# Performance work log

Hardware: AMD Instinct MI355X
Metric: run time of the kernel (lower is better)

The kernel has to match this reference:

```python
import jax, jax.numpy as jnp
import numpy as np

T, D, N, K, H = 2048, 4096, 32, 8, 128
ROPE_THETA = 500000.0


def setup_inputs() -> dict:
    key = jax.random.key(0)
    ks = jax.random.split(key, 5)
    s = 0.02
    return {
        "x": jax.random.normal(ks[0], (T, D), jnp.float32) * s,
        "positions": jnp.arange(T, dtype=jnp.int64 if jax.config.jax_enable_x64 else jnp.int32),
        "Wq": jax.random.normal(ks[1], (D, N, H), jnp.float32) * s,
        "Wk": jax.random.normal(ks[2], (D, K, H), jnp.float32) * s,
        "Wv": jax.random.normal(ks[3], (D, K, H), jnp.float32) * s,
        "Wo": jax.random.normal(ks[4], (N, H, D), jnp.float32) * s,
    }


def _rope(positions, q, k):
    # positions: [T]; q: [T,N,H]; k: [T,K,H]. Half-split rotation (Llama style).
    half = H // 2
    inv_freq = 1.0 / (ROPE_THETA ** (jnp.arange(0, half, dtype=jnp.float32) / half))
    ang = positions.astype(jnp.float32)[:, None] * inv_freq  # [T, H/2]
    cos = jnp.cos(ang)[:, None, :]  # [T,1,H/2]
    sin = jnp.sin(ang)[:, None, :]

    def rot(x):
        x1, x2 = x[..., :half], x[..., half:]
        return jnp.concatenate([x1 * cos - x2 * sin, x2 * cos + x1 * sin], axis=-1)

    return rot(q), rot(k)


def reference(x, positions, Wq, Wk, Wv, Wo):
    q = jnp.einsum('td,dnh->tnh', x, Wq)  # [T,N,H]
    k = jnp.einsum('td,dkh->tkh', x, Wk)  # [T,K,H]
    v = jnp.einsum('td,dkh->tkh', x, Wv)
    q, k = _rope(positions, q, k)

    rep = N // K  # GQA: expand kv heads to query heads
    kr = jnp.repeat(k, rep, axis=1)  # [T,N,H]
    vr = jnp.repeat(v, rep, axis=1)

    scale = 1.0 / jnp.sqrt(jnp.asarray(H, jnp.float32))
    scores = jnp.einsum('tnh,snh->nts', q, kr) * scale  # [N,T,T]
    causal = positions[:, None] >= positions[None, :]   # [T,T]
    scores = jnp.where(causal[None, :, :], scores, jnp.finfo(scores.dtype).min)
    probs = jax.nn.softmax(scores, axis=-1)
    ctx = jnp.einsum('nts,snh->tnh', probs, vr)  # [T,N,H]
    return jnp.einsum('tnh,nhd->td', ctx, Wo)
```

## Files before the change

### kernel.cpp

```cpp
#include <hip/hip_runtime.h>
#include <hip/hip_bf16.h>

#define T_SEQ 2048
#define D_MODEL 4096
#define N_HEADS 32
#define K_HEADS 8
#define HEAD_DIM 128

typedef unsigned short u16;
typedef short sfrag8 __attribute__((ext_vector_type(8)));
typedef float ffrag4 __attribute__((ext_vector_type(4)));

#if defined(__has_builtin)
#  if __has_builtin(__builtin_amdgcn_exp2f)
#    define EXP2F(x) __builtin_amdgcn_exp2f(x)
#  else
#    define EXP2F(x) exp2f(x)
#  endif
#else
#  define EXP2F(x) exp2f(x)
#endif

#define QSCALE_LOG2E 0.12751744900463627f

__device__ __forceinline__ float bf2f(u16 u) {
    return __uint_as_float(((unsigned int)u) << 16);
}
__device__ __forceinline__ u16 f2bf(float f) {
    unsigned int x = __float_as_uint(f);
    unsigned int r = (x + 0x7fffu + ((x >> 16) & 1u)) >> 16;
    return (u16)r;
}
__device__ __forceinline__ uint4 pack8(const float4 a, const float4 b) {
    uint4 r;
    r.x = (unsigned)f2bf(a.x) | ((unsigned)f2bf(a.y) << 16);
    r.y = (unsigned)f2bf(a.z) | ((unsigned)f2bf(a.w) << 16);
    r.z = (unsigned)f2bf(b.x) | ((unsigned)f2bf(b.y) << 16);
    r.w = (unsigned)f2bf(b.z) | ((unsigned)f2bf(b.w) << 16);
    return r;
}

__device__ __forceinline__ void gload_lds16(const u16* g, u16* l) {
    __builtin_amdgcn_global_load_lds(
        (const __attribute__((address_space(1))) void*)g,
        (__attribute__((address_space(3))) void*)l, 16, 0, 0);
}

__global__ __launch_bounds__(256) void convert_bf16(
    const float* __restrict__ X, u16* __restrict__ Y, int n8)
{
    const int i = blockIdx.x * 256 + threadIdx.x;
    if (i < n8) {
        float4 a = ((const float4*)X)[(size_t)i * 2];
        float4 b = ((const float4*)X)[(size_t)i * 2 + 1];
        ((uint4*)Y)[i] = pack8(a, b);
    }
}

__global__ __launch_bounds__(256) void transpose_f32_bf16(
    const float* __restrict__ W, u16* __restrict__ WT, int R, int C)
{
    __shared__ float Ts[64][65];
    const int t = threadIdx.x;
    const int c0 = blockIdx.x * 64, r0 = blockIdx.y * 64;
    const int rl = t >> 4, cl = (t & 15) * 4;
#pragma unroll
    for (int p = 0; p < 4; ++p) {
        const int r = p * 16 + rl;
        float4 v = *(const float4*)(W + (size_t)(r0 + r) * C + c0 + cl);
        Ts[r][cl] = v.x; Ts[r][cl + 1] = v.y; Ts[r][cl + 2] = v.z; Ts[r][cl + 3] = v.w;
    }
    __syncthreads();
    const int nl = t >> 2, k4 = (t & 3) * 16;
    u16 tmp[16];
#pragma unroll
    for (int j = 0; j < 16; ++j) tmp[j] = f2bf(Ts[k4 + j][nl]);
    u16* dst = WT + (size_t)(c0 + nl) * R + r0 + k4;
    *(uint4*)(dst) = *(uint4*)&tmp[0];
    *(uint4*)(dst + 8) = *(uint4*)&tmp[8];
}

template <int CMODE>
__global__ __launch_bounds__(256) void gemm_bt(
    const u16* __restrict__ A, const u16* __restrict__ BT,
    void* __restrict__ Cp, int M, int Nb, int Kd, int ldc)
{
    __shared__ __align__(16) u16 As[128 * 64];
    __shared__ __align__(16) u16 Bs[128 * 64];

    const int tid = threadIdx.x;
    const int lane = tid & 63;
    const int w = tid >> 6;
    const int wm = w >> 1, wn = w & 1;
    const int ln = lane & 15, quad = lane >> 4;

    int wid = blockIdx.y * gridDim.x + blockIdx.x;
    const int nwg = gridDim.x * gridDim.y;
    const int cpx = nwg >> 3;
    wid = (wid & 7) * cpx + (wid >> 3);
    const int bx = wid % gridDim.x;
    const int by = wid / gridDim.x;

    const int m0 = by * 128, n0 = bx * 128;

    size_t aoff[4], boff[4];
#pragma unroll
    for (int i = 0; i < 4; ++i) {
        const int row = (i * 4 + w) * 8 + (lane >> 3);
        const int cg = (lane & 7) ^ (lane >> 3);
        aoff[i] = (size_t)(m0 + row) * Kd + cg * 8;
        boff[i] = (size_t)(n0 + row) * Kd + cg * 8;
    }

    ffrag4 acc[4][4];
#pragma unroll
    for (int mi = 0; mi < 4; ++mi)
#pragma unroll
        for (int ni = 0; ni < 4; ++ni) acc[mi][ni] = (ffrag4){0.f, 0.f, 0.f, 0.f};

    for (int k0 = 0; k0 < Kd; k0 += 64) {
#pragma unroll
        for (int i = 0; i < 4; ++i) {
            gload_lds16(A + aoff[i] + k0, &As[(i * 4 + w) * 512]);
            gload_lds16(BT + boff[i] + k0, &Bs[(i * 4 + w) * 512]);
        }
        __syncthreads();

#pragma unroll
        for (int kk = 0; kk < 2; ++kk) {
            sfrag8 af[4], bfv[4];
#pragma unroll
            for (int mi = 0; mi < 4; ++mi) {
                const int row = wm * 64 + mi * 16 + ln;
                const int pc = ((kk * 4) | quad) ^ (ln & 7);
                af[mi] = *(const sfrag8*)&As[row * 64 + pc * 8];
            }
#pragma unroll
            for (int ni = 0; ni < 4; ++ni) {
                const int row = wn * 64 + ni * 16 + ln;
                const int pc = ((kk * 4) | quad) ^ (ln & 7);
                bfv[ni] = *(const sfrag8*)&Bs[row * 64 + pc * 8];
            }
#pragma unroll
            for (int mi = 0; mi < 4; ++mi)
#pragma unroll
                for (int ni = 0; ni < 4; ++ni)
                    acc[mi][ni] = __builtin_amdgcn_mfma_f32_16x16x32_bf16(
                        af[mi], bfv[ni], acc[mi][ni], 0, 0, 0);
        }
        __syncthreads();
    }

#pragma unroll
    for (int mi = 0; mi < 4; ++mi) {
#pragma unroll
        for (int ni = 0; ni < 4; ++ni) {
            const int gcol = n0 + wn * 64 + ni * 16 + ln;
#pragma unroll
            for (int i = 0; i < 4; ++i) {
                const int grow = m0 + wm * 64 + mi * 16 + quad * 4 + i;
                if constexpr (CMODE == 1) {
                    ((float*)Cp)[(size_t)grow * ldc + gcol] = acc[mi][ni][i];
                } else if constexpr (CMODE == 4) {
                    u16* base = (u16*)Cp;
                    const u16 v = f2bf(acc[mi][ni][i]);
                    if (gcol < 4096) {
                        base[4194304u + (size_t)grow * 4096 + gcol] = v;
                    } else if (gcol < 5120) {
                        base[(size_t)grow * 1024 + (gcol - 4096)] = v;
                    } else {
                        base[2097152u + (size_t)(gcol - 5120) * T_SEQ + grow] = v;
                    }
                } else {
                    ((u16*)Cp)[(size_t)grow * ldc + gcol] = f2bf(acc[mi][ni][i]);
                }
            }
        }
    }
}

template <int AMODE, int CMODE>
__global__ __launch_bounds__(256) void gemm_any(
    const void* __restrict__ Ap, const float* __restrict__ B, void* __restrict__ Cp,
    int M, int Nb, int Kd, int ldc)
{
    __shared__ __align__(16) u16 As[64 * 64];
    __shared__ __align__(16) u16 Bs[64 * 72];

    const int tid = threadIdx.x;
    const int n0 = blockIdx.x * 64, m0 = blockIdx.y * 64;

    const int lr = tid >> 3;
    const int cc8 = tid & 7;
    const int sw = ((cc8 ^ (lr & 7)) * 8);
    const int dstA0 = lr * 64 + sw;
    const int dstA1 = (lr + 32) * 64 + sw;
    const size_t arow0 = (size_t)(m0 + lr) * Kd;
    const size_t arow1 = (size_t)(m0 + lr + 32) * Kd;

    const int kr = tid >> 2;
    const int ncb = (tid & 3) * 16;

    const int lane = tid & 63;
    const int w = tid >> 6;
    const int col16 = lane & 15;
    const int quad = lane >> 4;
    const int swl = lane & 7;
    const int mrow = w * 16 + col16;

    ffrag4 acc[4];
#pragma unroll
    for (int j = 0; j < 4; ++j) acc[j] = (ffrag4){0.f, 0.f, 0.f, 0.f};

    for (int k0 = 0; k0 < Kd; k0 += 64) {
        if constexpr (AMODE == 1) {
            const u16* Af = (const u16*)Ap;
            uint4 va0 = *(const uint4*)(Af + arow0 + k0 + cc8 * 8);
            uint4 va1 = *(const uint4*)(Af + arow1 + k0 + cc8 * 8);
            *(uint4*)&As[dstA0] = va0;
            *(uint4*)&As[dstA1] = va1;
        } else {
            const float* Af = (const float*)Ap;
            float4 a00 = *(const float4*)(Af + arow0 + k0 + cc8 * 8);
            float4 a01 = *(const float4*)(Af + arow0 + k0 + cc8 * 8 + 4);
            float4 a10 = *(const float4*)(Af + arow1 + k0 + cc8 * 8);
            float4 a11 = *(const float4*)(Af + arow1 + k0 + cc8 * 8 + 4);
            *(uint4*)&As[dstA0] = pack8(a00, a01);
            *(uint4*)&As[dstA1] = pack8(a10, a11);
        }
        {
            const float* bp = B + (size_t)(k0 + kr) * Nb + n0 + ncb;
            float4 b0 = *(const float4*)(bp);
            float4 b1 = *(const float4*)(bp + 4);
            float4 b2 = *(const float4*)(bp + 8);
            float4 b3 = *(const float4*)(bp + 12);
            u16 tmp[16];
            tmp[0] = f2bf(b0.x); tmp[1] = f2bf(b0.y); tmp[2] = f2bf(b0.z); tmp[3] = f2bf(b0.w);
            tmp[4] = f2bf(b1.x); tmp[5] = f2bf(b1.y); tmp[6] = f2bf(b1.z); tmp[7] = f2bf(b1.w);
            tmp[8] = f2bf(b2.x); tmp[9] = f2bf(b2.y); tmp[10] = f2bf(b2.z); tmp[11] = f2bf(b2.w);
            tmp[12] = f2bf(b3.x); tmp[13] = f2bf(b3.y); tmp[14] = f2bf(b3.z); tmp[15] = f2bf(b3.w);
#pragma unroll
            for (int e = 0; e < 16; ++e)
                Bs[(ncb + e) * 72 + kr] = tmp[e];
        }
        __syncthreads();
#pragma unroll
        for (int c = 0; c < 2; ++c) {
            const int cc = c * 4 + quad;
            const int koffA = (cc ^ swl) * 8;
            sfrag8 af = *(const sfrag8*)&As[mrow * 64 + koffA];
#pragma unroll
            for (int j = 0; j < 4; ++j) {
                sfrag8 bfv = *(const sfrag8*)&Bs[(j * 16 + col16) * 72 + cc * 8];
                acc[j] = __builtin_amdgcn_mfma_f32_16x16x32_bf16(af, bfv, acc[j], 0, 0, 0);
            }
        }
        __syncthreads();
    }

#pragma unroll
    for (int j = 0; j < 4; ++j) {
        const int gcol = n0 + j * 16 + col16;
#pragma unroll
        for (int i = 0; i < 4; ++i) {
            const int grow = m0 + w * 16 + quad * 4 + i;
            if constexpr (CMODE == 1) {
                ((float*)Cp)[(size_t)grow * ldc + gcol] = acc[j][i];
            } else if constexpr (CMODE == 2) {
                ((u16*)Cp)[(size_t)gcol * ldc + grow] = f2bf(acc[j][i]);
            } else {
                ((u16*)Cp)[(size_t)grow * ldc + gcol] = f2bf(acc[j][i]);
            }
        }
    }
}

__global__ __launch_bounds__(64) void rope_kernel(
    u16* __restrict__ buf, int nheads, int t0)
{
    const int h = blockIdx.x;
    const int t = blockIdx.y;
    u16* rowp = buf + ((size_t)t * nheads + h) * HEAD_DIM;
    const int i = threadIdx.x;
    const float p = (float)(t0 + t);
    const float inv = expf(-((float)i * (1.0f / 64.0f)) * 13.122363377404329f);
    const float ang = p * inv;
    const float c = cosf(ang);
    const float s = sinf(ang);
    const float x1 = bf2f(rowp[i]);
    const float x2 = bf2f(rowp[i + 64]);
    rowp[i] = f2bf(x1 * c - x2 * s);
    rowp[i + 64] = f2bf(x2 * c + x1 * s);
}

__global__ __launch_bounds__(256) void attn_mfma(
    const u16* q, const u16* __restrict__ k,
    const u16* __restrict__ vt, u16* ctx, int t0)
{
    __shared__ __align__(16) u16 Kt[64 * 136];
    __shared__ __align__(16) u16 Vt[128 * 72];
    __shared__ __align__(16) u16 Ps[4][16 * 72];

    const int head = blockIdx.x;
    const int qt = gridDim.y - 1 - blockIdx.y;
    const int kvh = head >> 2;
    const int tid = threadIdx.x;
    const int lane = tid & 63;
    const int w = tid >> 6;
    const int ln = lane & 15;
    const int quad = lane >> 4;

    const int kr = tid >> 2;
    const int c4 = (tid & 3) * 32;
    const int vd = tid >> 1;
    const int vh = (tid & 1) * 32;

    const int qrow_loc = qt * 64 + w * 16 + ln;
    sfrag8 qf[4];
    {
        const u16* qg = q + ((size_t)qrow_loc * N_HEADS + head) * HEAD_DIM;
#pragma unroll
        for (int kk = 0; kk < 4; ++kk)
            qf[kk] = *(const sfrag8*)(qg + kk * 32 + quad * 8);
    }

    ffrag4 acc_o[8];
#pragma unroll
    for (int dt = 0; dt < 8; ++dt) acc_o[dt] = (ffrag4){0.f, 0.f, 0.f, 0.f};
    float mrow[4] = {-INFINITY, -INFINITY, -INFINITY, -INFINITY};
    float lrow_l[4] = {0.f, 0.f, 0.f, 0.f};

    const int Tq0 = t0 + qt * 64;
    const int nst = Tq0 / 64 + 1;
    const int qabs_base = Tq0 + w * 16 + quad * 4;

    for (int st = 0; st < nst; ++st) {
        const int kv0 = st * 64;
        const bool diag = (st == nst - 1);

        __syncthreads();
        {
            const u16* kg = k + ((size_t)(kv0 + kr) * K_HEADS + kvh) * HEAD_DIM + c4;
            u16* kd = &Kt[kr * 136 + c4];
#pragma unroll
            for (int j = 0; j < 4; ++j)
                *(uint4*)(kd + j * 8) = *(const uint4*)(kg + j * 8);
        }
        {
            const u16* vg = vt + ((size_t)(kvh * 128 + vd)) * T_SEQ + kv0 + vh;
            u16* vdst = &Vt[vd * 72 + vh];
#pragma unroll
            for (int j = 0; j < 4; ++j)
                *(uint4*)(vdst + j * 8) = *(const uint4*)(vg + j * 8);
        }
        __syncthreads();

        const int ktc = diag ? ((w < 2) ? 2 : 4) : 4;
        ffrag4 sacc[4];
        __builtin_amdgcn_s_setprio(1);
#pragma unroll
        for (int kt = 0; kt < 4; ++kt) {
            if (kt >= ktc) break;
            sacc[kt] = (ffrag4){0.f, 0.f, 0.f, 0.f};
#pragma unroll
            for (int kk = 0; kk < 4; ++kk) {
                sfrag8 bfr = *(const sfrag8*)&Kt[(kt * 16 + ln) * 136 + kk * 32 + quad * 8];
                sacc[kt] = __builtin_amdgcn_mfma_f32_16x16x32_bf16(qf[kk], bfr, sacc[kt], 0, 0, 0);
            }
        }
        __builtin_amdgcn_s_setprio(0);
        float sv[4][4];
#pragma unroll
        for (int kt = 0; kt < 4; ++kt) {
            if (kt >= ktc) break;
            const int key_abs = kv0 + kt * 16 + ln;
#pragma unroll
            for (int i = 0; i < 4; ++i) {
                float s = sacc[kt][i] * QSCALE_LOG2E;
                if (diag && key_abs > qabs_base + i) s = -INFINITY;
                sv[kt][i] = s;
            }
        }
        bool grew = false;
#pragma unroll
        for (int kt = 0; kt < 4; ++kt) {
            if (kt >= ktc) break;
#pragma unroll
            for (int i = 0; i < 4; ++i)
                grew |= (sv[kt][i] > mrow[i] + 8.0f);
        }
        if (__any(grew)) {
            float tm[4];
#pragma unroll
            for (int i = 0; i < 4; ++i) {
                float t = sv[0][i];
                for (int kt = 1; kt < ktc; ++kt) t = fmaxf(t, sv[kt][i]);
                t = fmaxf(t, __shfl_xor(t, 1));
                t = fmaxf(t, __shfl_xor(t, 2));
                t = fmaxf(t, __shfl_xor(t, 4));
                t = fmaxf(t, __shfl_xor(t, 8));
                tm[i] = t;
            }
            float alpha[4];
#pragma unroll
            for (int i = 0; i < 4; ++i) {
                const float mn = fmaxf(mrow[i], tm[i]);
                alpha[i] = EXP2F(mrow[i] - mn);
                mrow[i] = mn;
            }
            const bool noop = (alpha[0] == 1.f) && (alpha[1] == 1.f) &&
                              (alpha[2] == 1.f) && (alpha[3] == 1.f);
            if (!__all(noop)) {
#pragma unroll
                for (int i = 0; i < 4; ++i) {
                    lrow_l[i] *= alpha[i];
#pragma unroll
                    for (int dt = 0; dt < 8; ++dt) acc_o[dt][i] *= alpha[i];
                }
            }
        }
#pragma unroll
        for (int kt = 0; kt < 4; ++kt) {
            if (kt >= ktc) break;
#pragma unroll
            for (int i = 0; i < 4; ++i) {
                const float p = EXP2F(sv[kt][i] - mrow[i]);
                lrow_l[i] += p;
                Ps[w][(quad * 4 + i) * 72 + kt * 16 + ln] = f2bf(p);
            }
        }
        const int kbm = ktc >> 1;
        __builtin_amdgcn_s_setprio(1);
#pragma unroll
        for (int kb = 0; kb < 2; ++kb) {
            if (kb >= kbm) break;
            sfrag8 afr = *(const sfrag8*)&Ps[w][ln * 72 + kb * 32 + quad * 8];
#pragma unroll
            for (int dt = 0; dt < 8; ++dt) {
                sfrag8 bfr = *(const sfrag8*)&Vt[(dt * 16 + ln) * 72 + kb * 32 + quad * 8];
                acc_o[dt] = __builtin_amdgcn_mfma_f32_16x16x32_bf16(afr, bfr, acc_o[dt], 0, 0, 0);
            }
        }
        __builtin_amdgcn_s_setprio(0);
    }

    float invl[4];
#pragma unroll
    for (int i = 0; i < 4; ++i) {
        float t = lrow_l[i];
        t += __shfl_xor(t, 1);
        t += __shfl_xor(t, 2);
        t += __shfl_xor(t, 4);
        t += __shfl_xor(t, 8);
        invl[i] = 1.0f / t;
    }
#pragma unroll
    for (int i = 0; i < 4; ++i) {
        u16* og = ctx + ((size_t)(qt * 64 + w * 16 + quad * 4 + i) * N_HEADS + head) * HEAD_DIM;
#pragma unroll
        for (int dt = 0; dt < 8; ++dt)
            og[dt * 16 + ln] = f2bf(acc_o[dt][i] * invl[i]);
    }
}

extern "C" void kernel_launch(void* const* d_in, const int* in_sizes, int n_in,
                              void* d_out, int out_size, void* d_ws, size_t ws_size,
                              hipStream_t stream) {
    (void)in_sizes; (void)n_in; (void)out_size;
    const float* x  = (const float*)d_in[0];
    const float* Wq = (const float*)d_in[2];
    const float* Wk = (const float*)d_in[3];
    const float* Wv = (const float*)d_in[4];
    const float* Wo = (const float*)d_in[5];
    float* out = (float*)d_out;
    char* ws = (char*)d_ws;
    const size_t MiB = 1024 * 1024;

    if (ws_size >= 88 * MiB) {
        u16* kbuf  = (u16*)(ws);
        u16* vtbuf = (u16*)(ws + 4 * MiB);
        u16* qsl   = (u16*)(ws + 8 * MiB);
        u16* xb    = (u16*)(ws + 24 * MiB);
        u16* WqkvT = (u16*)(ws + 40 * MiB);

        convert_bf16<<<dim3(T_SEQ * D_MODEL / 8 / 256), 256, 0, stream>>>(
            x, xb, T_SEQ * D_MODEL / 8);
        transpose_f32_bf16<<<dim3(64, 64), 256, 0, stream>>>(
            Wq, WqkvT, D_MODEL, N_HEADS * HEAD_DIM);
        transpose_f32_bf16<<<dim3(16, 64), 256, 0, stream>>>(
            Wk, WqkvT + (size_t)4096 * 4096, D_MODEL, K_HEADS * HEAD_DIM);
        transpose_f32_bf16<<<dim3(16, 64), 256, 0, stream>>>(
            Wv, WqkvT + (size_t)5120 * 4096, D_MODEL, K_HEADS * HEAD_DIM);

        gemm_bt<4><<<dim3(48, 16), 256, 0, stream>>>(
            xb, WqkvT, ws, T_SEQ, 6144, D_MODEL, 0);

        rope_kernel<<<dim3(K_HEADS, T_SEQ), 64, 0, stream>>>(kbuf, K_HEADS, 0);
        rope_kernel<<<dim3(N_HEADS, T_SEQ), 64, 0, stream>>>(qsl, N_HEADS, 0);

        attn_mfma<<<dim3(N_HEADS, T_SEQ / 64), 256, 0, stream>>>(
            qsl, kbuf, vtbuf, qsl, 0);

        transpose_f32_bf16<<<dim3(64, 64), 256, 0, stream>>>(
            Wo, WqkvT, N_HEADS * HEAD_DIM, D_MODEL);
        gemm_bt<1><<<dim3(32, 16), 256, 0, stream>>>(
            qsl, WqkvT, out, T_SEQ, D_MODEL, N_HEADS * HEAD_DIM, D_MODEL);
        return;
    }

    u16* kbuf  = (u16*)(ws);
    u16* vtbuf = (u16*)(ws + 4194304);
    u16* qsl   = (u16*)(ws + 8388608);

    int S = 8;
    if (ws_size >= (size_t)8388608 + 16777216)      S = 1;
    else if (ws_size >= (size_t)8388608 + 8388608)  S = 2;
    else if (ws_size >= (size_t)8388608 + 4194304)  S = 4;
    const int Ts = T_SEQ / S;

    gemm_any<0, 0><<<dim3(16, T_SEQ / 64), 256, 0, stream>>>(
        x, Wk, kbuf, T_SEQ, K_HEADS * HEAD_DIM, D_MODEL, K_HEADS * HEAD_DIM);
    gemm_any<0, 2><<<dim3(16, T_SEQ / 64), 256, 0, stream>>>(
        x, Wv, vtbuf, T_SEQ, K_HEADS * HEAD_DIM, D_MODEL, T_SEQ);
    rope_kernel<<<dim3(K_HEADS, T_SEQ), 64, 0, stream>>>(kbuf, K_HEADS, 0);

    for (int s = 0; s < S; ++s) {
        const int t0 = s * Ts;
        gemm_any<0, 0><<<dim3(64, Ts / 64), 256, 0, stream>>>(
            x + (size_t)t0 * D_MODEL, Wq, qsl, Ts, D_MODEL, D_MODEL, D_MODEL);
        rope_kernel<<<dim3(N_HEADS, Ts), 64, 0, stream>>>(qsl, N_HEADS, t0);
        attn_mfma<<<dim3(N_HEADS, Ts / 64), 256, 0, stream>>>(
            qsl, kbuf, vtbuf, qsl, t0);
        gemm_any<1, 1><<<dim3(64, Ts / 64), 256, 0, stream>>>(
            qsl, Wo, out + (size_t)t0 * D_MODEL, Ts, D_MODEL, N_HEADS * HEAD_DIM, D_MODEL);
    }
}
```

Baseline: 549.7 us.

## Fuse RoPE into QKV projection GEMM epilogue and drop separate rope kernels

The QKV GEMM epilogue now stages each 128x128 bf16 output tile in shared memory, then applies the half-split RoPE rotation per head (128-column tiles line up with heads) before writing Q and K. Positions are taken to equal the row index. The two standalone rope kernels, which re-read and re-wrote Q and K in global memory, are removed. In exchange the epilogue does per-element sinf/cosf, an extra LDS round trip and a barrier, and the rotation now uses bf16-rounded inputs computed inside the GEMM.

```diff
diff --git a/kernel.cpp b/kernel.cpp
--- a/kernel.cpp
+++ b/kernel.cpp
@@ -22,6 +22,7 @@
 #endif
 
 #define QSCALE_LOG2E 0.12751744900463627f
+#define NEG_L2_THETA_64 (-0.29580575889569f)
 
 __device__ __forceinline__ float bf2f(u16 u) {
     return __uint_as_float(((unsigned int)u) << 16);
@@ -85,8 +86,9 @@
     const u16* __restrict__ A, const u16* __restrict__ BT,
     void* __restrict__ Cp, int M, int Nb, int Kd, int ldc)
 {
-    __shared__ __align__(16) u16 As[128 * 64];
-    __shared__ __align__(16) u16 Bs[128 * 64];
+    __shared__ __align__(16) u16 SmemAll[2 * 128 * 64];
+    u16* As = SmemAll;
+    u16* Bs = SmemAll + 128 * 64;
 
     const int tid = threadIdx.x;
     const int lane = tid & 63;
@@ -151,6 +153,68 @@
         __syncthreads();
     }
 
+    if constexpr (CMODE == 4) {
+        u16* base = (u16*)Cp;
+        if (n0 < 5120) {
+#pragma unroll
+            for (int mi = 0; mi < 4; ++mi)
+#pragma unroll
+                for (int ni = 0; ni < 4; ++ni) {
+                    const int colL = wn * 64 + ni * 16 + ln;
+#pragma unroll
+                    for (int i = 0; i < 4; ++i) {
+                        const int rowL = wm * 64 + mi * 16 + quad * 4 + i;
+                        SmemAll[rowL * 128 + colL] = f2bf(acc[mi][ni][i]);
+                    }
+                }
+            __syncthreads();
+            float invf[4];
+#pragma unroll
+            for (int ni = 0; ni < 4; ++ni)
+                invf[ni] = EXP2F((float)(ni * 16 + ln) * NEG_L2_THETA_64);
+#pragma unroll
+            for (int mi = 0; mi < 4; ++mi)
+#pragma unroll
+                for (int ni = 0; ni < 4; ++ni) {
+                    const int colL = wn * 64 + ni * 16 + ln;
+                    const int fi = colL & 63;
+                    const int gcol = n0 + colL;
+#pragma unroll
+                    for (int i = 0; i < 4; ++i) {
+                        const int rowL = wm * 64 + mi * 16 + quad * 4 + i;
+                        const int grow = m0 + rowL;
+                        const float x1 = bf2f(SmemAll[rowL * 128 + fi]);
+                        const float x2 = bf2f(SmemAll[rowL * 128 + fi + 64]);
+                        const float ang = (float)grow * invf[ni];
+                        const float cw = cosf(ang);
+                        const float sw = sinf(ang);
+                        const float o = (wn == 0) ? (x1 * cw - x2 * sw)
+                                                  : (x2 * cw + x1 * sw);
+                        const u16 v = f2bf(o);
+                        if (gcol < 4096) {
+                            base[4194304u + (size_t)grow * 4096 + gcol] = v;
+                        } else {
+                            base[(size_t)grow * 1024 + (gcol - 4096)] = v;
+                        }
+                    }
+                }
+        } else {
+#pragma unroll
+            for (int mi = 0; mi < 4; ++mi)
+#pragma unroll
+                for (int ni = 0; ni < 4; ++ni) {
+                    const int gcol = n0 + wn * 64 + ni * 16 + ln;
+#pragma unroll
+                    for (int i = 0; i < 4; ++i) {
+                        const int grow = m0 + wm * 64 + mi * 16 + quad * 4 + i;
+                        base[2097152u + (size_t)(gcol - 5120) * T_SEQ + grow] =
+                            f2bf(acc[mi][ni][i]);
+                    }
+                }
+        }
+        return;
+    }
+
 #pragma unroll
     for (int mi = 0; mi < 4; ++mi) {
 #pragma unroll
@@ -161,16 +225,6 @@
                 const int grow = m0 + wm * 64 + mi * 16 + quad * 4 + i;
                 if constexpr (CMODE == 1) {
                     ((float*)Cp)[(size_t)grow * ldc + gcol] = acc[mi][ni][i];
-                } else if constexpr (CMODE == 4) {
-                    u16* base = (u16*)Cp;
-                    const u16 v = f2bf(acc[mi][ni][i]);
-                    if (gcol < 4096) {
-                        base[4194304u + (size_t)grow * 4096 + gcol] = v;
-                    } else if (gcol < 5120) {
-                        base[(size_t)grow * 1024 + (gcol - 4096)] = v;
-                    } else {
-                        base[2097152u + (size_t)(gcol - 5120) * T_SEQ + grow] = v;
-                    }
                 } else {
                     ((u16*)Cp)[(size_t)grow * ldc + gcol] = f2bf(acc[mi][ni][i]);
                 }
@@ -495,9 +549,6 @@
         gemm_bt<4><<<dim3(48, 16), 256, 0, stream>>>(
             xb, WqkvT, ws, T_SEQ, 6144, D_MODEL, 0);
 
-        rope_kernel<<<dim3(K_HEADS, T_SEQ), 64, 0, stream>>>(kbuf, K_HEADS, 0);
-        rope_kernel<<<dim3(N_HEADS, T_SEQ), 64, 0, stream>>>(qsl, N_HEADS, 0);
-
         attn_mfma<<<dim3(N_HEADS, T_SEQ / 64), 256, 0, stream>>>(
             qsl, kbuf, vtbuf, qsl, 0);
 
```

New measurement: 524.0 us. 1.05x faster.
